# Kernel optimization log

Measured on AMD Instinct MI355X. Metric: run time of the kernel, lower is better.

Reference implementation:

```python
import jax, jax.numpy as jnp
import numpy as np

B, D, OUT = 256, 63, 128
DP = D + 1  # 64


def setup_inputs() -> dict:
    key = jax.random.key(0)
    k1, k2, k3, k4, k5 = jax.random.split(key, 5)
    return {
        "x": jax.random.normal(k1, (B, D), dtype=jnp.float32),
        "protein_output": jax.random.normal(k2, (B, D), dtype=jnp.float32),
        "dynamic_output": jax.random.normal(k3, (B, D), dtype=jnp.float32),
        "W": jax.random.normal(k4, (DP ** 3, OUT), dtype=jnp.float32) * 0.02,
        "b": jax.random.normal(k5, (OUT,), dtype=jnp.float32) * 0.02,
    }


def reference(x, protein_output, dynamic_output, W, b):
    bsz = x.shape[0]
    ones = jnp.ones((bsz, 1), dtype=x.dtype)
    a = jnp.concatenate([x, ones], axis=1)               # [B, D+1]
    p = jnp.concatenate([protein_output, ones], axis=1)   # [B, D+1]
    d = jnp.concatenate([dynamic_output, ones], axis=1)   # [B, D+1]
    # rank-1 trilinear outer product, flattened row-major: idx = (i*(D+1)+j)*(D+1)+k
    ab = jnp.einsum('bi,bj->bij', a, p)                   # [B, D+1, D+1]
    abc = jnp.einsum('bij,bk->bijk', ab, d)               # [B, D+1, D+1, D+1]
    feat = abc.reshape(bsz, -1)                           # [B, (D+1)^3]
    return feat @ W + b                                   # [B, OUT]
```

## Files before the change

kernel.cpp:

```cpp
#include <hip/hip_runtime.h>
#include <hip/hip_bf16.h>

typedef __attribute__((ext_vector_type(8))) short short8v;
typedef __attribute__((ext_vector_type(4))) float floatx4;
typedef __attribute__((ext_vector_type(4))) unsigned int uint4v;

union FragU { uint4v u4; unsigned int u[4]; short8v v; };

__device__ __forceinline__ unsigned int pkbf(float a, float b) {
  __hip_bfloat162 h = __float22bfloat162_rn(make_float2(a, b));
  union { __hip_bfloat162 h; unsigned int u; } c; c.h = h;
  return c.u;
}

__global__ void bias_init(const float* __restrict__ bias, float* __restrict__ out) {
  int idx = blockIdx.x * 256 + threadIdx.x;
  out[idx] = bias[idx & 127];
}

__global__ __launch_bounds__(512)
void reduce_v6(const float* __restrict__ part, const float* __restrict__ bias,
               float* __restrict__ out) {
  const int tid = threadIdx.x;
  const int col = tid & 127;
  const int qr = tid >> 7;
  const int b = blockIdx.x;

  const float* pp = part + (long)(qr * 128 + (col >> 5)) * 8192
                    + b * 32 + (col & 31);
  float s0 = 0.f, s1 = 0.f, s2 = 0.f, s3 = 0.f;
  #pragma unroll 4
  for (int n = 0; n < 32; n += 4) {
    s0 += __builtin_nontemporal_load(pp + (long)n * 32768);
    s1 += __builtin_nontemporal_load(pp + (long)(n + 1) * 32768);
    s2 += __builtin_nontemporal_load(pp + (long)(n + 2) * 32768);
    s3 += __builtin_nontemporal_load(pp + (long)(n + 3) * 32768);
  }
  float sum = (s0 + s1) + (s2 + s3);

  __shared__ float red[3][128];
  if (qr) red[qr - 1][col] = sum;
  __syncthreads();
  if (qr == 0)
    out[b * 128 + col] = sum + red[0][col] + red[1][col] + red[2][col] + bias[col];
}

__global__ __launch_bounds__(512, 4)
void tfn_gemm_v6(const float* __restrict__ X, const float* __restrict__ P,
                 const float* __restrict__ Dyn, const float* __restrict__ W,
                 float* __restrict__ part) {
  __shared__ unsigned int wlds[4][1024];
  __shared__ float p_lds[32][257];

  const int tid = threadIdx.x;
  const int wv = tid >> 6, lane = tid & 63;
  const int q = lane >> 4, l16 = lane & 15;

  const int bx = blockIdx.x;
  const int ig = bx >> 3;
  const int jh = (bx >> 2) & 1;
  const int cq = bx & 3;

  const int pr = tid >> 3, cc = tid & 7;
  const float* wbase = W + ((long)ig << 19) + ((long)jh << 18)
                       + (cq << 5) + (cc << 2) + (long)pr * 256;

  floatx4 rg0 = __builtin_nontemporal_load((const floatx4*)wbase);
  floatx4 rg1 = __builtin_nontemporal_load((const floatx4*)(wbase + 128));

  #pragma unroll
  for (int it = 0; it < 16; ++it) {
    int idx = tid + (it << 9);
    int jj = idx & 31, bb = idx >> 5;
    int j = (jh << 5) + jj;
    p_lds[jj][bb] = (j < 63) ? P[bb * 63 + j] : 1.0f;
  }

  float e[2][2][8];
  #pragma unroll
  for (int rt = 0; rt < 2; ++rt) {
    int brow = (wv << 5) + (rt << 4) + l16;
    float av = (ig < 63) ? X[brow * 63 + ig] : 1.0f;
    #pragma unroll
    for (int h = 0; h < 2; ++h) {
      int kb = (h << 5) + (q << 3);
      #pragma unroll
      for (int t = 0; t < 8; ++t) {
        int k = kb + t;
        float dv = (k < 63) ? Dyn[brow * 63 + k] : 1.0f;
        e[rt][h][t] = av * dv;
      }
    }
  }

  const int wtile0 = pr >> 5;
  const int wpr = pr & 31;
  const int wcol = cc << 2;

  {
    unsigned int* tb = &wlds[wtile0][0];
    #pragma unroll
    for (int w = 0; w < 4; ++w) {
      int col = wcol + w;
      tb[((col << 5) + wpr) ^ ((col & 7) << 2)] = pkbf(rg0[w], rg1[w]);
    }
  }
  rg0 = __builtin_nontemporal_load((const floatx4*)(wbase + (1 << 14)));
  rg1 = __builtin_nontemporal_load((const floatx4*)(wbase + (1 << 14) + 128));

  int roff[2][2];
  #pragma unroll
  for (int nt = 0; nt < 2; ++nt) {
    int col = (nt << 4) + l16;
    #pragma unroll
    for (int h = 0; h < 2; ++h)
      roff[nt][h] = (col << 5) + (((h << 4) + (q << 2)) ^ ((col & 7) << 2));
  }
  const int prow = (wv << 5) + l16;

  floatx4 acc[2][2];
  #pragma unroll
  for (int a = 0; a < 2; ++a)
    #pragma unroll
    for (int b = 0; b < 2; ++b) acc[a][b] = (floatx4)0.0f;

  __syncthreads();

  for (int dt = 0; dt < 16; ++dt) {
    if (dt < 15) {
      unsigned int* tb = &wlds[(((dt + 1) & 1) << 1) + wtile0][0];
      #pragma unroll
      for (int w = 0; w < 4; ++w) {
        int col = wcol + w;
        tb[((col << 5) + wpr) ^ ((col & 7) << 2)] = pkbf(rg0[w], rg1[w]);
      }
      if (dt < 14) {
        rg0 = __builtin_nontemporal_load((const floatx4*)(wbase + ((long)(dt + 2) << 14)));
        rg1 = __builtin_nontemporal_load((const floatx4*)(wbase + ((long)(dt + 2) << 14) + 128));
      }
    }

    #pragma unroll
    for (int jj2 = 0; jj2 < 2; ++jj2) {
      int jl = (dt << 1) + jj2;
      const unsigned int* tb = &wlds[((dt & 1) << 1) + jj2][0];
      float pbv[2];
      pbv[0] = p_lds[jl][prow];
      pbv[1] = p_lds[jl][prow + 16];

      #pragma unroll
      for (int h = 0; h < 2; ++h) {
        FragU fb[2], fa[2];
        #pragma unroll
        for (int nt = 0; nt < 2; ++nt)
          fb[nt].u4 = *(const uint4v*)(tb + roff[nt][h]);
        #pragma unroll
        for (int rt = 0; rt < 2; ++rt)
          #pragma unroll
          for (int v2 = 0; v2 < 4; ++v2)
            fa[rt].u[v2] = pkbf(pbv[rt] * e[rt][h][2 * v2],
                                pbv[rt] * e[rt][h][2 * v2 + 1]);
        #pragma unroll
        for (int rt = 0; rt < 2; ++rt)
          #pragma unroll
          for (int nt = 0; nt < 2; ++nt)
            acc[rt][nt] = __builtin_amdgcn_mfma_f32_16x16x32_bf16(
                fa[rt].v, fb[nt].v, acc[rt][nt], 0, 0, 0);
      }
    }
    if (dt < 15) __syncthreads();
  }

  float* pt = part + ((long)bx << 13);
  #pragma unroll
  for (int rt = 0; rt < 2; ++rt)
    #pragma unroll
    for (int nt = 0; nt < 2; ++nt) {
      int cl = (nt << 4) + l16;
      #pragma unroll
      for (int g = 0; g < 4; ++g) {
        int row = (wv << 5) + (rt << 4) + (q << 2) + g;
        pt[row * 32 + cl] = acc[rt][nt][g];
      }
    }
}

__global__ __launch_bounds__(512, 2)
void tfn_gemm(const float* __restrict__ X, const float* __restrict__ P,
              const float* __restrict__ Dyn, const float* __restrict__ W,
              float* __restrict__ out) {
  __shared__ float p_lds[16][256];

  const int tid = threadIdx.x;
  const int wv = tid >> 6, lane = tid & 63;
  const int q = lane >> 4, l16 = lane & 15;
  const int r = wv & 3;
  const int cg = wv >> 2;

  const int c = blockIdx.x;
  const int i = c >> 2;
  const int j0 = (c & 3) << 4;
  const long gk0 = (long)c << 10;

  for (int idx = tid; idx < 256 * 16; idx += 512) {
    int bb = idx >> 4, jj = idx & 15;
    int j = j0 + jj;
    p_lds[jj][bb] = (j < 63) ? P[bb * 63 + j] : 1.0f;
  }

  float e[4][2][8];
  #pragma unroll
  for (int rt = 0; rt < 4; ++rt) {
    int brow = (r << 6) + (rt << 4) + l16;
    float av = (i < 63) ? X[brow * 63 + i] : 1.0f;
    #pragma unroll
    for (int h = 0; h < 2; ++h) {
      int kb = (h << 5) + (q << 3);
      #pragma unroll
      for (int t = 0; t < 8; ++t) {
        int k = kb + t;
        float dv = (k < 63) ? Dyn[brow * 63 + k] : 1.0f;
        e[rt][h][t] = av * dv;
      }
    }
  }

  floatx4 acc[4][4];
  #pragma unroll
  for (int a = 0; a < 4; ++a)
    #pragma unroll
    for (int b = 0; b < 4; ++b) acc[a][b] = (floatx4)0.0f;

  __syncthreads();

  const float* wstep = W + (gk0 + (q << 3)) * 128 + (cg << 6) + l16;

  float wA[4][8], wB[4][8];
  #pragma unroll
  for (int nt = 0; nt < 4; ++nt)
    #pragma unroll
    for (int t = 0; t < 8; ++t)
      wA[nt][t] = wstep[t * 128 + nt * 16];

  for (int jj = 0; jj < 16; ++jj) {
    float pb[4];
    #pragma unroll
    for (int rt = 0; rt < 4; ++rt)
      pb[rt] = p_lds[jj][(r << 6) + (rt << 4) + l16];

    {
      const float* wp = wstep + ((long)(2 * jj + 1) << 12);
      #pragma unroll
      for (int nt = 0; nt < 4; ++nt)
        #pragma unroll
        for (int t = 0; t < 8; ++t)
          wB[nt][t] = wp[t * 128 + nt * 16];

      union { short8v v; unsigned int u[4]; } fb[4], fa[4];
      #pragma unroll
      for (int nt = 0; nt < 4; ++nt)
        #pragma unroll
        for (int v2 = 0; v2 < 4; ++v2)
          fb[nt].u[v2] = pkbf(wA[nt][2 * v2], wA[nt][2 * v2 + 1]);
      #pragma unroll
      for (int rt = 0; rt < 4; ++rt)
        #pragma unroll
        for (int v2 = 0; v2 < 4; ++v2)
          fa[rt].u[v2] = pkbf(pb[rt] * e[rt][0][2 * v2], pb[rt] * e[rt][0][2 * v2 + 1]);
      #pragma unroll
      for (int rt = 0; rt < 4; ++rt)
        #pragma unroll
        for (int nt = 0; nt < 4; ++nt)
          acc[rt][nt] = __builtin_amdgcn_mfma_f32_16x16x32_bf16(
              fa[rt].v, fb[nt].v, acc[rt][nt], 0, 0, 0);
    }

    {
      if (jj < 15) {
        const float* wp = wstep + ((long)(2 * jj + 2) << 12);
        #pragma unroll
        for (int nt = 0; nt < 4; ++nt)
          #pragma unroll
          for (int t = 0; t < 8; ++t)
            wA[nt][t] = wp[t * 128 + nt * 16];
      }

      union { short8v v; unsigned int u[4]; } fb[4], fa[4];
      #pragma unroll
      for (int nt = 0; nt < 4; ++nt)
        #pragma unroll
        for (int v2 = 0; v2 < 4; ++v2)
          fb[nt].u[v2] = pkbf(wB[nt][2 * v2], wB[nt][2 * v2 + 1]);
      #pragma unroll
      for (int rt = 0; rt < 4; ++rt)
        #pragma unroll
        for (int v2 = 0; v2 < 4; ++v2)
          fa[rt].u[v2] = pkbf(pb[rt] * e[rt][1][2 * v2], pb[rt] * e[rt][1][2 * v2 + 1]);
      #pragma unroll
      for (int rt = 0; rt < 4; ++rt)
        #pragma unroll
        for (int nt = 0; nt < 4; ++nt)
          acc[rt][nt] = __builtin_amdgcn_mfma_f32_16x16x32_bf16(
              fa[rt].v, fb[nt].v, acc[rt][nt], 0, 0, 0);
    }
  }

  #pragma unroll
  for (int rt = 0; rt < 4; ++rt)
    #pragma unroll
    for (int nt = 0; nt < 4; ++nt) {
      int col = (cg << 6) + (nt << 4) + l16;
      #pragma unroll
      for (int g = 0; g < 4; ++g) {
        int brow = (r << 6) + (rt << 4) + (q << 2) + g;
        atomicAdd(&out[brow * 128 + col], acc[rt][nt][g]);
      }
    }
}

extern "C" void kernel_launch(void* const* d_in, const int* in_sizes, int n_in,
                              void* d_out, int out_size, void* d_ws, size_t ws_size,
                              hipStream_t stream) {
  const float* x   = (const float*)d_in[0];
  const float* p   = (const float*)d_in[1];
  const float* dyn = (const float*)d_in[2];
  const float* W   = (const float*)d_in[3];
  const float* b   = (const float*)d_in[4];
  float* out = (float*)d_out;

  const size_t part_bytes = (size_t)512 * 8192 * sizeof(float);

  if (d_ws != nullptr && ws_size >= part_bytes) {
    float* part = (float*)d_ws;
    tfn_gemm_v6<<<512, 512, 0, stream>>>(x, p, dyn, W, part);
    reduce_v6<<<256, 512, 0, stream>>>(part, b, out);
  } else {
    bias_init<<<128, 256, 0, stream>>>(b, out);
    tfn_gemm<<<256, 512, 0, stream>>>(x, p, dyn, W, out);
  }
}
```

Baseline: 210.4 us.

## Deepen W staging pipeline to triple LDS buffers with two register stages

Replaces the double-buffered LDS staging of W tiles with a three-slot LDS ring, and keeps two register sets of global loads in flight so each load is issued four iterations before its tile is consumed. The aim is to hide HBM latency on the streaming W read, which dominates this memory-bound GEMM. The cost is extra LDS (about 8 KB more per block), which may reduce occupancy at 4 blocks per CU, and more live registers.

```diff
diff --git a/kernel.cpp b/kernel.cpp
--- a/kernel.cpp
+++ b/kernel.cpp
@@ -46,10 +46,10 @@
 }
 
 __global__ __launch_bounds__(512, 4)
-void tfn_gemm_v6(const float* __restrict__ X, const float* __restrict__ P,
+void tfn_gemm_v7(const float* __restrict__ X, const float* __restrict__ P,
                  const float* __restrict__ Dyn, const float* __restrict__ W,
                  float* __restrict__ part) {
-  __shared__ unsigned int wlds[4][1024];
+  __shared__ unsigned int wlds[6][1024];
   __shared__ float p_lds[32][257];
 
   const int tid = threadIdx.x;
@@ -65,8 +65,26 @@
   const float* wbase = W + ((long)ig << 19) + ((long)jh << 18)
                        + (cq << 5) + (cc << 2) + (long)pr * 256;
 
-  floatx4 rg0 = __builtin_nontemporal_load((const floatx4*)wbase);
-  floatx4 rg1 = __builtin_nontemporal_load((const floatx4*)(wbase + 128));
+  const int wtile0 = pr >> 5;
+  const int wpr = pr & 31;
+  const int wcol = cc << 2;
+
+  auto ldw = [&](int dt, floatx4& r0, floatx4& r1) {
+    r0 = __builtin_nontemporal_load((const floatx4*)(wbase + ((long)dt << 14)));
+    r1 = __builtin_nontemporal_load((const floatx4*)(wbase + ((long)dt << 14) + 128));
+  };
+  auto stage_write = [&](int slot, const floatx4& a, const floatx4& b) {
+    unsigned int* tb = &wlds[(slot << 1) + wtile0][0];
+    #pragma unroll
+    for (int w = 0; w < 4; ++w) {
+      int col = wcol + w;
+      tb[((col << 5) + wpr) ^ ((col & 7) << 2)] = pkbf(a[w], b[w]);
+    }
+  };
+
+  floatx4 rgA0, rgA1, rgB0, rgB1;
+  ldw(0, rgA0, rgA1);
+  ldw(1, rgB0, rgB1);
 
   #pragma unroll
   for (int it = 0; it < 16; ++it) {
@@ -93,20 +111,10 @@
     }
   }
 
-  const int wtile0 = pr >> 5;
-  const int wpr = pr & 31;
-  const int wcol = cc << 2;
-
-  {
-    unsigned int* tb = &wlds[wtile0][0];
-    #pragma unroll
-    for (int w = 0; w < 4; ++w) {
-      int col = wcol + w;
-      tb[((col << 5) + wpr) ^ ((col & 7) << 2)] = pkbf(rg0[w], rg1[w]);
-    }
-  }
-  rg0 = __builtin_nontemporal_load((const floatx4*)(wbase + (1 << 14)));
-  rg1 = __builtin_nontemporal_load((const floatx4*)(wbase + (1 << 14) + 128));
+  stage_write(0, rgA0, rgA1);
+  ldw(2, rgA0, rgA1);
+  stage_write(1, rgB0, rgB1);
+  ldw(3, rgB0, rgB1);
 
   int roff[2][2];
   #pragma unroll
@@ -126,24 +134,23 @@
 
   __syncthreads();
 
+  int csl = 0;
   for (int dt = 0; dt < 16; ++dt) {
-    if (dt < 15) {
-      unsigned int* tb = &wlds[(((dt + 1) & 1) << 1) + wtile0][0];
-      #pragma unroll
-      for (int w = 0; w < 4; ++w) {
-        int col = wcol + w;
-        tb[((col << 5) + wpr) ^ ((col & 7) << 2)] = pkbf(rg0[w], rg1[w]);
-      }
-      if (dt < 14) {
-        rg0 = __builtin_nontemporal_load((const floatx4*)(wbase + ((long)(dt + 2) << 14)));
-        rg1 = __builtin_nontemporal_load((const floatx4*)(wbase + ((long)(dt + 2) << 14) + 128));
+    int wsl = csl + 2; if (wsl >= 3) wsl -= 3;
+    if (dt < 14) {
+      if (dt & 1) {
+        stage_write(wsl, rgB0, rgB1);
+        if (dt < 12) ldw(dt + 4, rgB0, rgB1);
+      } else {
+        stage_write(wsl, rgA0, rgA1);
+        if (dt < 12) ldw(dt + 4, rgA0, rgA1);
       }
     }
 
     #pragma unroll
     for (int jj2 = 0; jj2 < 2; ++jj2) {
       int jl = (dt << 1) + jj2;
-      const unsigned int* tb = &wlds[((dt & 1) << 1) + jj2][0];
+      const unsigned int* tb = &wlds[(csl << 1) + jj2][0];
       float pbv[2];
       pbv[0] = p_lds[jl][prow];
       pbv[1] = p_lds[jl][prow + 16];
@@ -169,6 +176,7 @@
       }
     }
     if (dt < 15) __syncthreads();
+    csl += 1; if (csl == 3) csl = 0;
   }
 
   float* pt = part + ((long)bx << 13);
@@ -332,7 +340,7 @@
 
   if (d_ws != nullptr && ws_size >= part_bytes) {
     float* part = (float*)d_ws;
-    tfn_gemm_v6<<<512, 512, 0, stream>>>(x, p, dyn, W, part);
+    tfn_gemm_v7<<<512, 512, 0, stream>>>(x, p, dyn, W, part);
     reduce_v6<<<256, 512, 0, stream>>>(part, b, out);
   } else {
     bias_init<<<128, 256, 0, stream>>>(b, out);
```

Result: slower. 216.3 us (+2.8%).
